# Performance work log

Measured on AMD Instinct MI355X. Metric: run time of the kernel, lower is better.

The kernel has to match this reference:

```python
import jax, jax.numpy as jnp
import numpy as np

B, M, N = 4, 1024, 4096
DQ, DC, H, DH = 512, 512, 8, 64
D = H * DH
NEG = -10000000.0


def setup_inputs() -> dict:
    key = jax.random.key(0)
    ks = jax.random.split(key, 7)
    left = jax.random.normal(ks[0], (B, M, DQ), dtype=jnp.float32)
    right = jax.random.normal(ks[1], (B, N, DC), dtype=jnp.float32)
    mask = jax.random.randint(ks[2], (B, M, N), 0, 2).astype(bool)
    # learned params (torch Linear stores weight as (out,in); we store (in,out))
    Wq = jax.random.normal(ks[3], (DQ, D), dtype=jnp.float32) * (DQ ** -0.5)
    Wkv = jax.random.normal(ks[4], (DC, 2 * D), dtype=jnp.float32) * (DC ** -0.5)
    Wout = jax.random.normal(ks[5], (D, DQ), dtype=jnp.float32) * (D ** -0.5)
    bout = jax.random.normal(ks[6], (DQ,), dtype=jnp.float32) * 0.01
    return {"left": left, "right": right, "mask": mask,
            "Wq": Wq, "Wkv": Wkv, "Wout": Wout, "bout": bout}


def reference(left, right, mask, Wq, Wkv, Wout, bout):
    scale = DH ** -0.5
    q = left @ Wq                      # (B, M, D)
    kv = right @ Wkv                   # (B, N, 2D)
    k, v = jnp.split(kv, 2, axis=-1)   # (B, N, D) each
    q = q.reshape(B, M, H, DH).transpose(0, 2, 1, 3)  # (B, H, M, DH)
    k = k.reshape(B, N, H, DH).transpose(0, 2, 1, 3)  # (B, H, N, DH)
    v = v.reshape(B, N, H, DH).transpose(0, 2, 1, 3)  # (B, H, N, DH)
    sim = scale * jnp.einsum('bhmd,bhnd->bhmn', q, k)  # (B, H, M, N)
    sim = jnp.where(mask[:, None, :, :], sim, NEG)
    attn = jax.nn.softmax(sim, axis=-1)
    out = jnp.einsum('bhmn,bhnd->bhmd', attn, v)       # (B, H, M, DH)
    out = out.transpose(0, 2, 1, 3).reshape(B, M, D)
    return out @ Wout + bout           # (B, M, DQ)
```

## Files before the change

kernel.cpp:

```cpp
#include <hip/hip_runtime.h>

typedef _Float16 f16;
typedef __attribute__((ext_vector_type(8))) _Float16 half8;
typedef __attribute__((ext_vector_type(4))) _Float16 half4;
typedef __attribute__((ext_vector_type(4))) float floatx4;
typedef unsigned int uint32;
typedef __attribute__((ext_vector_type(4))) uint32 uint4v;

#define MFMA16(a, b, c) __builtin_amdgcn_mfma_f32_16x16x32_f16((a), (b), (c), 0, 0, 0)

constexpr int B_ = 4, M_ = 1024, N_ = 4096, DQ_ = 512, DC_ = 512, H_ = 8, DH_ = 64, D_ = 512;
constexpr int KP_ = 576;
constexpr int VP_ = 4224;
constexpr int NSPLIT = 4;
constexpr float QSC_ = 0.18033688011112042f;

typedef __attribute__((address_space(1))) const void glds_g;
typedef __attribute__((address_space(3))) void glds_l;
__device__ __forceinline__ void g2lds16(const void* g, void* l) {
    __builtin_amdgcn_global_load_lds((glds_g*)g, (glds_l*)l, 16, 0, 0);
}

__device__ __forceinline__ void wtr_tile(const float* __restrict__ src, f16* __restrict__ dst,
                                         int Nout, int bx, int by, int tid) {
    __shared__ __align__(16) f16 Ts[64][72];
    const int n0 = bx * 64, k0 = by * 64;
    {
        int kr = tid >> 2, q4 = tid & 3;
        const float* sp = src + (size_t)(k0 + kr) * Nout + n0 + q4 * 16;
        float4 x0 = *(const float4*)(sp + 0), x1 = *(const float4*)(sp + 4);
        float4 x2 = *(const float4*)(sp + 8), x3 = *(const float4*)(sp + 12);
        half8 h0, h1;
        h0[0]=(f16)x0.x; h0[1]=(f16)x0.y; h0[2]=(f16)x0.z; h0[3]=(f16)x0.w;
        h0[4]=(f16)x1.x; h0[5]=(f16)x1.y; h0[6]=(f16)x1.z; h0[7]=(f16)x1.w;
        h1[0]=(f16)x2.x; h1[1]=(f16)x2.y; h1[2]=(f16)x2.z; h1[3]=(f16)x2.w;
        h1[4]=(f16)x3.x; h1[5]=(f16)x3.y; h1[6]=(f16)x3.z; h1[7]=(f16)x3.w;
        *(half8*)&Ts[kr][q4 * 16] = h0;
        *(half8*)&Ts[kr][q4 * 16 + 8] = h1;
    }
    __syncthreads();
    {
        int nr = tid >> 2, q = tid & 3;
        half8 h0, h1;
#pragma unroll
        for (int j = 0; j < 8; j++) { h0[j] = Ts[q * 16 + j][nr]; h1[j] = Ts[q * 16 + 8 + j][nr]; }
        f16* dp = dst + (size_t)(n0 + nr) * 512 + k0 + q * 16;
        *(half8*)(dp + 0) = h0;
        *(half8*)(dp + 8) = h1;
    }
}

__global__ __launch_bounds__(256)
void prep_k(const void* __restrict__ mask, uint32* __restrict__ bits,
            const float* __restrict__ left, f16* __restrict__ leftb,
            const float* __restrict__ right, f16* __restrict__ rightb,
            const float* __restrict__ Wq, f16* __restrict__ wqt,
            const float* __restrict__ Wkv, f16* __restrict__ wkvt,
            const float* __restrict__ Wout, f16* __restrict__ woutt) {
    const int blk = blockIdx.x, tid = threadIdx.x;
    if (blk < 4096) {
        __shared__ int s_bad;
        if (tid == 0) s_bad = 0;
        __syncthreads();
        const uint32* w = (const uint32*)mask + (size_t)blk * 1024;
        int bad = 0;
#pragma unroll
        for (int j = 0; j < 4; j++) bad |= (w[tid * 4 + j] & 0xFFFFFFFEu) != 0u;
        if (bad) s_bad = 1;
        __syncthreads();
        const bool bytes_mode = s_bad != 0;
        uint32 v = 0;
        if (bytes_mode) {
            uint4 x = *(const uint4*)((const unsigned char*)mask + (size_t)blk * 4096 + tid * 16);
            uint32 ws_[4] = {x.x, x.y, x.z, x.w};
#pragma unroll
            for (int k = 0; k < 4; k++)
#pragma unroll
                for (int bb = 0; bb < 4; bb++)
                    v |= (((ws_[k] >> (8 * bb)) & 0xFFu) != 0u ? 1u : 0u) << (k * 4 + bb);
        } else {
            const uint4* p = (const uint4*)((const uint32*)mask + (size_t)blk * 4096 + tid * 16);
            uint4 x0 = p[0], x1 = p[1], x2 = p[2], x3 = p[3];
            uint32 ws_[16] = {x0.x, x0.y, x0.z, x0.w, x1.x, x1.y, x1.z, x1.w,
                              x2.x, x2.y, x2.z, x2.w, x3.x, x3.y, x3.z, x3.w};
#pragma unroll
            for (int k = 0; k < 16; k++) v |= (ws_[k] != 0u ? 1u : 0u) << k;
        }
        uint32 other = (uint32)__shfl_xor((int)v, 1);
        if ((tid & 1) == 0)
            bits[(size_t)blk * 128 + (tid >> 1)] = v | (other << 16);
    } else if (blk < 6144) {
        int i = ((blk - 4096) * 256 + tid) * 4;
        float4 x = *(const float4*)(left + i);
        half4 h; h[0] = (f16)x.x; h[1] = (f16)x.y; h[2] = (f16)x.z; h[3] = (f16)x.w;
        *(half4*)(leftb + i) = h;
    } else if (blk < 14336) {
        int i = ((blk - 6144) * 256 + tid) * 4;
        float4 x = *(const float4*)(right + i);
        half4 h; h[0] = (f16)x.x; h[1] = (f16)x.y; h[2] = (f16)x.z; h[3] = (f16)x.w;
        *(half4*)(rightb + i) = h;
    } else if (blk < 14400) {
        int r = blk - 14336;
        wtr_tile(Wq, wqt, 512, r & 7, r >> 3, tid);
    } else if (blk < 14528) {
        int r = blk - 14400;
        wtr_tile(Wkv, wkvt, 1024, r & 15, r >> 4, tid);
    } else {
        int r = blk - 14528;
        wtr_tile(Wout, woutt, 512, r & 7, r >> 3, tid);
    }
}

__global__ __launch_bounds__(256)
void gemmqkv_k(const f16* __restrict__ leftb, const f16* __restrict__ wqt,
               const f16* __restrict__ rightb, const f16* __restrict__ wkvt,
               f16* __restrict__ qb, f16* __restrict__ kb, f16* __restrict__ vt) {
    __shared__ __align__(16) f16 As[128 * 64];
    __shared__ __align__(16) f16 Bs[128 * 64];
    const int hw = blockIdx.x, tid = threadIdx.x;
    const int lane = tid & 63, wave = tid >> 6;
    const int qd = lane >> 4, l16 = lane & 15;
    const int wm = wave >> 1, wn = wave & 1;

    int mode;
    const f16* A; const f16* Bt; size_t m0, n0;
    if (hw < 1024) {
        const int xcd = hw & 7, slot = hw >> 3;
        const int mi_ = xcd * 16 + (slot & 15);
        const int ni_ = slot >> 4;
        size_t rows = (size_t)mi_ * 128, cols = (size_t)ni_ * 128;
        if (cols < 512) { mode = 0; A = rightb; m0 = rows; Bt = wkvt;   n0 = cols; }
        else            { mode = 1; A = wkvt;   m0 = cols; Bt = rightb; n0 = rows; }
    } else {
        const int r = hw - 1024;
        const int xcd = r & 7, slot = r >> 3;
        const int mi_ = xcd * 4 + (slot & 3);
        const int ni_ = slot >> 2;
        mode = 2; A = leftb; Bt = wqt;
        m0 = (size_t)mi_ * 128; n0 = (size_t)ni_ * 128;
    }

    size_t goff[4];
    f16 *la[4], *lb[4];
#pragma unroll
    for (int i = 0; i < 4; i++) {
        int c = i * 256 + wave * 64 + lane;
        int row = c >> 3, col8 = (c & 7) ^ (row & 7);
        goff[i] = (size_t)row * 512 + col8 * 8;
        la[i] = As + (size_t)(i * 256 + wave * 64) * 8;
        lb[i] = Bs + (size_t)(i * 256 + wave * 64) * 8;
    }
    const f16* Ab = A + m0 * 512;
    const f16* Bb = Bt + n0 * 512;

    floatx4 acc[4][4] = {};

    for (int k0 = 0; k0 < 512; k0 += 64) {
        __syncthreads();
#pragma unroll
        for (int i = 0; i < 4; i++) g2lds16(Ab + goff[i] + k0, la[i]);
#pragma unroll
        for (int i = 0; i < 4; i++) g2lds16(Bb + goff[i] + k0, lb[i]);
        __syncthreads();
#pragma unroll
        for (int kk = 0; kk < 2; kk++) {
            half8 a[4], b[4];
#pragma unroll
            for (int t = 0; t < 4; t++) {
                int rowa = wm * 64 + t * 16 + l16;
                int rowb = wn * 64 + t * 16 + l16;
                int pa8 = ((kk * 4 + qd) ^ (rowa & 7)) * 8;
                int pb8 = ((kk * 4 + qd) ^ (rowb & 7)) * 8;
                a[t] = *(const half8*)&As[rowa * 64 + pa8];
                b[t] = *(const half8*)&Bs[rowb * 64 + pb8];
            }
#pragma unroll
            for (int mt = 0; mt < 4; mt++)
#pragma unroll
                for (int nt = 0; nt < 4; nt++)
                    acc[mt][nt] = MFMA16(a[mt], b[nt], acc[mt][nt]);
        }
    }

#pragma unroll
    for (int mt = 0; mt < 4; mt++)
#pragma unroll
        for (int nt = 0; nt < 4; nt++)
#pragma unroll
            for (int r = 0; r < 4; r++) {
                size_t mi = m0 + wm * 64 + mt * 16 + qd * 4 + r;
                size_t ni = n0 + wn * 64 + nt * 16 + l16;
                float v = acc[mt][nt][r];
                if (mode == 2) {
                    qb[mi * 512 + ni] = (f16)v;
                } else if (mode == 0) {
                    kb[mi * KP_ + ni] = (f16)v;
                } else {
                    int dcol = (int)mi - 512;
                    int hh = dcol >> 6, dh = dcol & 63;
                    size_t bb = ni >> 12, nn = ni & 4095;
                    vt[((bb * H_ + hh) * (size_t)DH_ + dh) * VP_ + nn] = (f16)v;
                }
            }
}

__global__ __launch_bounds__(512, 8)
void attn_k(const f16* __restrict__ Qb, const f16* __restrict__ Kb,
            const f16* __restrict__ Vt, const uint32* __restrict__ mb,
            float* __restrict__ Op, float* __restrict__ Lp) {
    const int tid = threadIdx.x;
    const int lane = tid & 63, wave = tid >> 6;
    const int qd = lane >> 4, l16 = lane & 15;
    const int bh = blockIdx.x, b = bh >> 3, h = bh & 7;
    const int z = blockIdx.z;
    constexpr int iters = N_ / (64 * NSPLIT);
    const int n_base = z * iters * 64;
    const int m_base = blockIdx.y * 128 + wave * 16;

    __shared__ __align__(16) f16 Ks[2][64 * 64];
    __shared__ __align__(16) f16 Vs[2][64 * 64];

    half8 q0, q1;
    {
        const f16* qrow = Qb + ((size_t)(b * M_ + m_base + l16)) * D_ + h * DH_;
        half8 r0 = *(const half8*)(qrow + qd * 8);
        half8 r1 = *(const half8*)(qrow + 32 + qd * 8);
#pragma unroll
        for (int j = 0; j < 8; j++) {
            q0[j] = (f16)((float)r0[j] * QSC_);
            q1[j] = (f16)((float)r1[j] * QSC_);
        }
    }

    floatx4 ot[4] = {};
    float l_acc = 0.0f;

    const uint32* mrow = mb + ((size_t)(b * M_ + m_base + l16)) * (N_ / 32);

    const int srow = wave * 8;
    const int r8 = lane >> 3, p8 = lane & 7;
    const int gc8 = p8 ^ r8;
    const f16* kg = Kb + ((size_t)(b * N_) + srow + r8) * KP_ + h * DH_ + gc8 * 8;
    const f16* vg = Vt + ((size_t)(bh * DH_) + srow + r8) * VP_ + gc8 * 8;

    auto stage = [&](int buf, int n0) {
        g2lds16(kg + (size_t)n0 * KP_, &Ks[buf][srow * 64]);
        g2lds16(vg + n0, &Vs[buf][srow * 64]);
    };

    stage(0, n_base);
    uint2 mmc = *(const uint2*)(mrow + (n_base >> 5));
    int cur = 0;

    const int swz = (l16 & 7);
    const int c0 = (qd ^ swz) * 8;
    const int c1 = ((4 + qd) ^ swz) * 8;

    for (int it = 0; it < iters; it++) {
        const int n0 = n_base + it * 64;
        __syncthreads();
        uint2 mmn;
        if (it + 1 < iters) {
            stage(cur ^ 1, n0 + 64);
            mmn = *(const uint2*)(mrow + ((n0 + 64) >> 5));
        }
        const f16* Kc = &Ks[cur][0];
        const f16* Vc = &Vs[cur][0];

        const uint32 u0 = mmc.x >> (qd * 4);
        const uint32 u1 = mmc.y >> (qd * 4);

        uint32 pk[4][2];
        half8 kc0 = *(const half8*)&Kc[(l16) * 64 + c0];
        half8 kc1 = *(const half8*)&Kc[(l16) * 64 + c1];
#pragma unroll
        for (int s = 0; s < 4; s++) {
            floatx4 t = {};
            t = MFMA16(kc0, q0, t);
            t = MFMA16(kc1, q1, t);
            if (s < 3) {
                const int ro = ((s + 1) * 16 + l16) * 64;
                kc0 = *(const half8*)&Kc[ro + c0];
                kc1 = *(const half8*)&Kc[ro + c1];
            }
            uint32 us = (s & 2 ? u1 : u0) >> ((s & 1) * 16);
            float e0 = __builtin_amdgcn_exp2f(t[0]);
            float e1 = __builtin_amdgcn_exp2f(t[1]);
            float e2 = __builtin_amdgcn_exp2f(t[2]);
            float e3 = __builtin_amdgcn_exp2f(t[3]);
            e0 = (us & 1u) ? e0 : 0.0f;
            e1 = (us & 2u) ? e1 : 0.0f;
            e2 = (us & 4u) ? e2 : 0.0f;
            e3 = (us & 8u) ? e3 : 0.0f;
            l_acc += (e0 + e1) + (e2 + e3);
            pk[s][0] = __builtin_bit_cast(uint32, __builtin_amdgcn_cvt_pkrtz(e0, e1));
            pk[s][1] = __builtin_bit_cast(uint32, __builtin_amdgcn_cvt_pkrtz(e2, e3));
        }

        half8 pa[2];
#pragma unroll
        for (int hh = 0; hh < 2; hh++) {
            uint32 w0, w1, w2, w3;
            {
                auto a = __builtin_amdgcn_permlane32_swap(pk[2 * hh][0], pk[2 * hh + 1][0], false, false);
                auto c = __builtin_amdgcn_permlane16_swap(a[0], a[1], false, false);
                w0 = c[0]; w2 = c[1];
            }
            {
                auto a = __builtin_amdgcn_permlane32_swap(pk[2 * hh][1], pk[2 * hh + 1][1], false, false);
                auto c = __builtin_amdgcn_permlane16_swap(a[0], a[1], false, false);
                w1 = c[0]; w3 = c[1];
            }
            uint4v wv = {w0, w1, w2, w3};
            pa[hh] = __builtin_bit_cast(half8, wv);
        }

        half8 vc0 = *(const half8*)&Vc[(l16) * 64 + c0];
        half8 vc1 = *(const half8*)&Vc[(l16) * 64 + c1];
#pragma unroll
        for (int sd = 0; sd < 4; sd++) {
            floatx4 o = ot[sd];
            o = MFMA16(vc0, pa[0], o);
            o = MFMA16(vc1, pa[1], o);
            if (sd < 3) {
                const int ro = ((sd + 1) * 16 + l16) * 64;
                vc0 = *(const half8*)&Vc[ro + c0];
                vc1 = *(const half8*)&Vc[ro + c1];
            }
            ot[sd] = o;
        }
        mmc = mmn;
        cur ^= 1;
    }

    l_acc += __shfl_xor(l_acc, 16);
    l_acc += __shfl_xor(l_acc, 32);

    {
        size_t row = (size_t)(z * 32 + bh) * M_ + m_base + l16;
        float* op = Op + row * DH_ + qd * 4;
#pragma unroll
        for (int sd = 0; sd < 4; sd++)
            __builtin_nontemporal_store(ot[sd], (floatx4*)(op + sd * 16));
        if (qd == 0) __builtin_nontemporal_store(l_acc, Lp + row);
    }
}

__global__ __launch_bounds__(256)
void comb_k(const float* __restrict__ Op, const float* __restrict__ Lp, f16* __restrict__ Ob,
            int nsp) {
    int i = blockIdx.x * 256 + threadIdx.x;
    int d4 = i & 15, m = (i >> 4) & 1023, bh = i >> 14;
    float nx = 0.f, ny = 0.f, nz = 0.f, nw = 0.f, den = 0.f;
    for (int s = 0; s < nsp; s++) {
        size_t row = ((size_t)s * 32 + bh) * M_ + m;
        float4 x = *(const float4*)(Op + row * DH_ + d4 * 4);
        nx += x.x; ny += x.y; nz += x.z; nw += x.w;
        den += Lp[row];
    }
    float r = 1.0f / den;
    int b = bh >> 3, h = bh & 7;
    f16* o = Ob + ((size_t)(b * M_ + m)) * D_ + h * DH_ + d4 * 4;
    half4 hv; hv[0] = (f16)(nx * r); hv[1] = (f16)(ny * r); hv[2] = (f16)(nz * r); hv[3] = (f16)(nw * r);
    *(half4*)o = hv;
}

__global__ __launch_bounds__(256)
void gemmout_k(const f16* __restrict__ A, const f16* __restrict__ Bt,
               float* __restrict__ Fout, const float* __restrict__ bias) {
    __shared__ __align__(16) f16 As[2][64 * 64];
    __shared__ __align__(16) f16 Bs[2][64 * 64];
    const int tid = threadIdx.x;
    const int lane = tid & 63, wave = tid >> 6;
    const int qd = lane >> 4, l16 = lane & 15;
    const int wm = wave >> 1, wn = wave & 1;
    const size_t m0 = (size_t)blockIdx.x * 64;
    const size_t n0 = (size_t)blockIdx.y * 64;

    size_t goff[2];
    f16 *la[2][2], *lb[2][2];
#pragma unroll
    for (int i = 0; i < 2; i++) {
        int c = i * 256 + wave * 64 + lane;
        int row = c >> 3, col8 = (c & 7) ^ (row & 7);
        goff[i] = (size_t)row * 512 + col8 * 8;
        la[0][i] = &As[0][(size_t)(i * 256 + wave * 64) * 8];
        la[1][i] = &As[1][(size_t)(i * 256 + wave * 64) * 8];
        lb[0][i] = &Bs[0][(size_t)(i * 256 + wave * 64) * 8];
        lb[1][i] = &Bs[1][(size_t)(i * 256 + wave * 64) * 8];
    }
    const f16* Ab = A + m0 * 512;
    const f16* Bb = Bt + n0 * 512;

    floatx4 acc[2][2] = {};

#pragma unroll
    for (int i = 0; i < 2; i++) g2lds16(Ab + goff[i], la[0][i]);
#pragma unroll
    for (int i = 0; i < 2; i++) g2lds16(Bb + goff[i], lb[0][i]);
    int cur = 0;

    for (int k0 = 0; k0 < 512; k0 += 64) {
        __syncthreads();
        if (k0 + 64 < 512) {
            const int nxt = cur ^ 1;
#pragma unroll
            for (int i = 0; i < 2; i++) g2lds16(Ab + goff[i] + k0 + 64, la[nxt][i]);
#pragma unroll
            for (int i = 0; i < 2; i++) g2lds16(Bb + goff[i] + k0 + 64, lb[nxt][i]);
        }
        const f16* Ac = &As[cur][0];
        const f16* Bc = &Bs[cur][0];
#pragma unroll
        for (int kk = 0; kk < 2; kk++) {
            half8 a[2], b[2];
#pragma unroll
            for (int t = 0; t < 2; t++) {
                int rowa = wm * 32 + t * 16 + l16;
                int rowb = wn * 32 + t * 16 + l16;
                int pa8 = ((kk * 4 + qd) ^ (rowa & 7)) * 8;
                int pb8 = ((kk * 4 + qd) ^ (rowb & 7)) * 8;
                a[t] = *(const half8*)&Ac[rowa * 64 + pa8];
                b[t] = *(const half8*)&Bc[rowb * 64 + pb8];
            }
#pragma unroll
            for (int mt = 0; mt < 2; mt++)
#pragma unroll
                for (int nt = 0; nt < 2; nt++)
                    acc[mt][nt] = MFMA16(a[mt], b[nt], acc[mt][nt]);
        }
        cur ^= 1;
    }

#pragma unroll
    for (int mt = 0; mt < 2; mt++)
#pragma unroll
        for (int nt = 0; nt < 2; nt++)
#pragma unroll
            for (int r = 0; r < 4; r++) {
                size_t row = m0 + wm * 32 + mt * 16 + qd * 4 + r;
                size_t col = n0 + wn * 32 + nt * 16 + l16;
                Fout[row * 512 + col] = acc[mt][nt][r] + bias[col];
            }
}

extern "C" void kernel_launch(void* const* d_in, const int* in_sizes, int n_in,
                              void* d_out, int out_size, void* d_ws, size_t ws_size,
                              hipStream_t stream) {
    const float* left  = (const float*)d_in[0];
    const float* right = (const float*)d_in[1];
    const void*  mask  = d_in[2];
    const float* Wq    = (const float*)d_in[3];
    const float* Wkv   = (const float*)d_in[4];
    const float* Wout  = (const float*)d_in[5];
    const float* bout  = (const float*)d_in[6];

    char* ws = (char*)d_ws;
    size_t off = 0;
    auto take = [&](size_t bytes) { char* p = ws + off; off += (bytes + 255) & ~(size_t)255; return p; };
    uint32* mbits = (uint32*)take((size_t)B_ * M_ * N_ / 8);
    f16* woutt = (f16*)take((size_t)D_ * DQ_ * 2);
    f16* qb    = (f16*)take((size_t)B_ * M_ * D_ * 2);
    f16* kb    = (f16*)take((size_t)B_ * N_ * KP_ * 2);
    f16* vt    = (f16*)take((size_t)B_ * H_ * DH_ * VP_ * 2);
    f16* ob    = (f16*)take((size_t)B_ * M_ * D_ * 2);
    char* pool = (char*)take((size_t)34 * 1024 * 1024);
    f16* leftb  = (f16*)pool;
    f16* rightb = (f16*)(pool + (size_t)4 * 1024 * 1024);
    f16* wqt    = (f16*)(pool + (size_t)20 * 1024 * 1024);
    f16* wkvt   = (f16*)(pool + (size_t)21 * 1024 * 1024);
    float* Op   = (float*)pool;
    float* Lp   = (float*)(pool + (size_t)NSPLIT * 32 * M_ * DH_ * 4);

    prep_k<<<14592, 256, 0, stream>>>(mask, mbits, left, leftb, right, rightb,
                                      Wq, wqt, Wkv, wkvt, Wout, woutt);
    gemmqkv_k<<<1152, 256, 0, stream>>>(leftb, wqt, rightb, wkvt, qb, kb, vt);
    attn_k<<<dim3(32, 8, NSPLIT), 512, 0, stream>>>(qb, kb, vt, mbits, Op, Lp);
    comb_k<<<2048, 256, 0, stream>>>(Op, Lp, ob, NSPLIT);
    gemmout_k<<<dim3(64, 8), 256, 0, stream>>>(ob, woutt, (float*)d_out, bout);
}
```

Baseline: 274.9 us.

## Process two 16-row query tiles per wave to reuse K/V LDS fragments

Each wave in the attention kernel now handles 32 query rows as two 16-row fragments instead of 16. Every K and V fragment read from LDS feeds twice as many MFMAs. The grid's M dimension is halved so each block covers 256 rows. This cuts LDS traffic and global K/V staging per query row. In exchange it roughly doubles accumulator and P registers per wave, lowers the launch-bounds occupancy hint from 8 to 4, and halves the number of blocks, which may reduce latency hiding.

```diff
diff --git a/kernel.cpp b/kernel.cpp
--- a/kernel.cpp
+++ b/kernel.cpp
@@ -204,7 +204,7 @@
             }
 }
 
-__global__ __launch_bounds__(512, 8)
+__global__ __launch_bounds__(512, 4)
 void attn_k(const f16* __restrict__ Qb, const f16* __restrict__ Kb,
             const f16* __restrict__ Vt, const uint32* __restrict__ mb,
             float* __restrict__ Op, float* __restrict__ Lp) {
@@ -215,27 +215,29 @@
     const int z = blockIdx.z;
     constexpr int iters = N_ / (64 * NSPLIT);
     const int n_base = z * iters * 64;
-    const int m_base = blockIdx.y * 128 + wave * 16;
+    const int m_base = blockIdx.y * 256 + wave * 32;
 
     __shared__ __align__(16) f16 Ks[2][64 * 64];
     __shared__ __align__(16) f16 Vs[2][64 * 64];
 
-    half8 q0, q1;
-    {
-        const f16* qrow = Qb + ((size_t)(b * M_ + m_base + l16)) * D_ + h * DH_;
+    half8 q[2][2];
+#pragma unroll
+    for (int f = 0; f < 2; f++) {
+        const f16* qrow = Qb + ((size_t)(b * M_ + m_base + f * 16 + l16)) * D_ + h * DH_;
         half8 r0 = *(const half8*)(qrow + qd * 8);
         half8 r1 = *(const half8*)(qrow + 32 + qd * 8);
 #pragma unroll
         for (int j = 0; j < 8; j++) {
-            q0[j] = (f16)((float)r0[j] * QSC_);
-            q1[j] = (f16)((float)r1[j] * QSC_);
-        }
-    }
-
-    floatx4 ot[4] = {};
-    float l_acc = 0.0f;
-
-    const uint32* mrow = mb + ((size_t)(b * M_ + m_base + l16)) * (N_ / 32);
+            q[f][0][j] = (f16)((float)r0[j] * QSC_);
+            q[f][1][j] = (f16)((float)r1[j] * QSC_);
+        }
+    }
+
+    floatx4 ot[2][4] = {};
+    float la0 = 0.0f, la1 = 0.0f;
+
+    const uint32* mrow0 = mb + ((size_t)(b * M_ + m_base + l16)) * (N_ / 32);
+    const uint32* mrow1 = mrow0 + (size_t)16 * (N_ / 32);
 
     const int srow = wave * 8;
     const int r8 = lane >> 3, p8 = lane & 7;
@@ -249,7 +251,8 @@
     };
 
     stage(0, n_base);
-    uint2 mmc = *(const uint2*)(mrow + (n_base >> 5));
+    uint2 mc0 = *(const uint2*)(mrow0 + (n_base >> 5));
+    uint2 mc1 = *(const uint2*)(mrow1 + (n_base >> 5));
     int cur = 0;
 
     const int swz = (l16 & 7);
@@ -259,90 +262,107 @@
     for (int it = 0; it < iters; it++) {
         const int n0 = n_base + it * 64;
         __syncthreads();
-        uint2 mmn;
+        uint2 mn0, mn1;
         if (it + 1 < iters) {
             stage(cur ^ 1, n0 + 64);
-            mmn = *(const uint2*)(mrow + ((n0 + 64) >> 5));
+            mn0 = *(const uint2*)(mrow0 + ((n0 + 64) >> 5));
+            mn1 = *(const uint2*)(mrow1 + ((n0 + 64) >> 5));
         }
         const f16* Kc = &Ks[cur][0];
         const f16* Vc = &Vs[cur][0];
 
-        const uint32 u0 = mmc.x >> (qd * 4);
-        const uint32 u1 = mmc.y >> (qd * 4);
-
-        uint32 pk[4][2];
-        half8 kc0 = *(const half8*)&Kc[(l16) * 64 + c0];
-        half8 kc1 = *(const half8*)&Kc[(l16) * 64 + c1];
+        const uint32 u00 = mc0.x >> (qd * 4), u01 = mc0.y >> (qd * 4);
+        const uint32 u10 = mc1.x >> (qd * 4), u11 = mc1.y >> (qd * 4);
+
+        uint32 pk[2][4][2];
 #pragma unroll
         for (int s = 0; s < 4; s++) {
-            floatx4 t = {};
-            t = MFMA16(kc0, q0, t);
-            t = MFMA16(kc1, q1, t);
-            if (s < 3) {
-                const int ro = ((s + 1) * 16 + l16) * 64;
-                kc0 = *(const half8*)&Kc[ro + c0];
-                kc1 = *(const half8*)&Kc[ro + c1];
-            }
-            uint32 us = (s & 2 ? u1 : u0) >> ((s & 1) * 16);
-            float e0 = __builtin_amdgcn_exp2f(t[0]);
-            float e1 = __builtin_amdgcn_exp2f(t[1]);
-            float e2 = __builtin_amdgcn_exp2f(t[2]);
-            float e3 = __builtin_amdgcn_exp2f(t[3]);
-            e0 = (us & 1u) ? e0 : 0.0f;
-            e1 = (us & 2u) ? e1 : 0.0f;
-            e2 = (us & 4u) ? e2 : 0.0f;
-            e3 = (us & 8u) ? e3 : 0.0f;
-            l_acc += (e0 + e1) + (e2 + e3);
-            pk[s][0] = __builtin_bit_cast(uint32, __builtin_amdgcn_cvt_pkrtz(e0, e1));
-            pk[s][1] = __builtin_bit_cast(uint32, __builtin_amdgcn_cvt_pkrtz(e2, e3));
-        }
-
-        half8 pa[2];
-#pragma unroll
-        for (int hh = 0; hh < 2; hh++) {
-            uint32 w0, w1, w2, w3;
+            const int ro = (s * 16 + l16) * 64;
+            half8 k0 = *(const half8*)&Kc[ro + c0];
+            half8 k1 = *(const half8*)&Kc[ro + c1];
             {
-                auto a = __builtin_amdgcn_permlane32_swap(pk[2 * hh][0], pk[2 * hh + 1][0], false, false);
-                auto c = __builtin_amdgcn_permlane16_swap(a[0], a[1], false, false);
-                w0 = c[0]; w2 = c[1];
+                floatx4 t = {};
+                t = MFMA16(k0, q[0][0], t);
+                t = MFMA16(k1, q[0][1], t);
+                uint32 us = (s & 2 ? u01 : u00) >> ((s & 1) * 16);
+                float e0 = __builtin_amdgcn_exp2f(t[0]);
+                float e1 = __builtin_amdgcn_exp2f(t[1]);
+                float e2 = __builtin_amdgcn_exp2f(t[2]);
+                float e3 = __builtin_amdgcn_exp2f(t[3]);
+                e0 = (us & 1u) ? e0 : 0.0f;
+                e1 = (us & 2u) ? e1 : 0.0f;
+                e2 = (us & 4u) ? e2 : 0.0f;
+                e3 = (us & 8u) ? e3 : 0.0f;
+                la0 += (e0 + e1) + (e2 + e3);
+                pk[0][s][0] = __builtin_bit_cast(uint32, __builtin_amdgcn_cvt_pkrtz(e0, e1));
+                pk[0][s][1] = __builtin_bit_cast(uint32, __builtin_amdgcn_cvt_pkrtz(e2, e3));
             }
             {
-                auto a = __builtin_amdgcn_permlane32_swap(pk[2 * hh][1], pk[2 * hh + 1][1], false, false);
-                auto c = __builtin_amdgcn_permlane16_swap(a[0], a[1], false, false);
-                w1 = c[0]; w3 = c[1];
-            }
-            uint4v wv = {w0, w1, w2, w3};
-            pa[hh] = __builtin_bit_cast(half8, wv);
-        }
-
-        half8 vc0 = *(const half8*)&Vc[(l16) * 64 + c0];
-        half8 vc1 = *(const half8*)&Vc[(l16) * 64 + c1];
+                floatx4 t = {};
+                t = MFMA16(k0, q[1][0], t);
+                t = MFMA16(k1, q[1][1], t);
+                uint32 us = (s & 2 ? u11 : u10) >> ((s & 1) * 16);
+                float e0 = __builtin_amdgcn_exp2f(t[0]);
+                float e1 = __builtin_amdgcn_exp2f(t[1]);
+                float e2 = __builtin_amdgcn_exp2f(t[2]);
+                float e3 = __builtin_amdgcn_exp2f(t[3]);
+                e0 = (us & 1u) ? e0 : 0.0f;
+                e1 = (us & 2u) ? e1 : 0.0f;
+                e2 = (us & 4u) ? e2 : 0.0f;
+                e3 = (us & 8u) ? e3 : 0.0f;
+                la1 += (e0 + e1) + (e2 + e3);
+                pk[1][s][0] = __builtin_bit_cast(uint32, __builtin_amdgcn_cvt_pkrtz(e0, e1));
+                pk[1][s][1] = __builtin_bit_cast(uint32, __builtin_amdgcn_cvt_pkrtz(e2, e3));
+            }
+        }
+
+        half8 pa[2][2];
+#pragma unroll
+        for (int f = 0; f < 2; f++)
+#pragma unroll
+            for (int hh = 0; hh < 2; hh++) {
+                uint32 w0, w1, w2, w3;
+                {
+                    auto a = __builtin_amdgcn_permlane32_swap(pk[f][2 * hh][0], pk[f][2 * hh + 1][0], false, false);
+                    auto c = __builtin_amdgcn_permlane16_swap(a[0], a[1], false, false);
+                    w0 = c[0]; w2 = c[1];
+                }
+                {
+                    auto a = __builtin_amdgcn_permlane32_swap(pk[f][2 * hh][1], pk[f][2 * hh + 1][1], false, false);
+                    auto c = __builtin_amdgcn_permlane16_swap(a[0], a[1], false, false);
+                    w1 = c[0]; w3 = c[1];
+                }
+                uint4v wv = {w0, w1, w2, w3};
+                pa[f][hh] = __builtin_bit_cast(half8, wv);
+            }
+
 #pragma unroll
         for (int sd = 0; sd < 4; sd++) {
-            floatx4 o = ot[sd];
-            o = MFMA16(vc0, pa[0], o);
-            o = MFMA16(vc1, pa[1], o);
-            if (sd < 3) {
-                const int ro = ((sd + 1) * 16 + l16) * 64;
-                vc0 = *(const half8*)&Vc[ro + c0];
-                vc1 = *(const half8*)&Vc[ro + c1];
-            }
-            ot[sd] = o;
-        }
-        mmc = mmn;
+            const int ro = (sd * 16 + l16) * 64;
+            half8 v0 = *(const half8*)&Vc[ro + c0];
+            half8 v1 = *(const half8*)&Vc[ro + c1];
+            ot[0][sd] = MFMA16(v0, pa[0][0], ot[0][sd]);
+            ot[0][sd] = MFMA16(v1, pa[0][1], ot[0][sd]);
+            ot[1][sd] = MFMA16(v0, pa[1][0], ot[1][sd]);
+            ot[1][sd] = MFMA16(v1, pa[1][1], ot[1][sd]);
+        }
+        mc0 = mn0; mc1 = mn1;
         cur ^= 1;
     }
 
-    l_acc += __shfl_xor(l_acc, 16);
-    l_acc += __shfl_xor(l_acc, 32);
-
-    {
-        size_t row = (size_t)(z * 32 + bh) * M_ + m_base + l16;
+    la0 += __shfl_xor(la0, 16);
+    la0 += __shfl_xor(la0, 32);
+    la1 += __shfl_xor(la1, 16);
+    la1 += __shfl_xor(la1, 32);
+
+#pragma unroll
+    for (int f = 0; f < 2; f++) {
+        size_t row = (size_t)(z * 32 + bh) * M_ + m_base + f * 16 + l16;
         float* op = Op + row * DH_ + qd * 4;
 #pragma unroll
         for (int sd = 0; sd < 4; sd++)
-            __builtin_nontemporal_store(ot[sd], (floatx4*)(op + sd * 16));
-        if (qd == 0) __builtin_nontemporal_store(l_acc, Lp + row);
+            __builtin_nontemporal_store(ot[f][sd], (floatx4*)(op + sd * 16));
+        if (qd == 0) __builtin_nontemporal_store(f == 0 ? la0 : la1, Lp + row);
     }
 }
 
@@ -475,7 +495,7 @@
     prep_k<<<14592, 256, 0, stream>>>(mask, mbits, left, leftb, right, rightb,
                                       Wq, wqt, Wkv, wkvt, Wout, woutt);
     gemmqkv_k<<<1152, 256, 0, stream>>>(leftb, wqt, rightb, wkvt, qb, kb, vt);
-    attn_k<<<dim3(32, 8, NSPLIT), 512, 0, stream>>>(qb, kb, vt, mbits, Op, Lp);
+    attn_k<<<dim3(32, 4, NSPLIT), 512, 0, stream>>>(qb, kb, vt, mbits, Op, Lp);
     comb_k<<<2048, 256, 0, stream>>>(Op, Lp, ob, NSPLIT);
     gemmout_k<<<dim3(64, 8), 256, 0, stream>>>(ob, woutt, (float*)d_out, bout);
 }
```

Measured after the change: 273.6 us. Within noise of the previous version (-0.5%).

## Fuse fp32-to-fp16 activation conversion into QKV GEMM with register prefetch

Applied to the files above, without the earlier changes.

Drops the separate conversion passes that wrote fp16 copies of left and right in the prep kernel. The QKV GEMM now reads fp32 activations directly, converts them in registers and writes them into LDS, prefetching the next K-slice into registers while the MFMAs run. It also remaps the block-to-tile assignment for the KV part and simplifies the attention kernel's K/V LDS loads by removing manual software prefetch. This saves a full write and read of the fp16 activation buffers, but doubles the global bytes read for the fp32 operand per GEMM tile and adds register pressure.

```diff
diff --git a/kernel.cpp b/kernel.cpp
--- a/kernel.cpp
+++ b/kernel.cpp
@@ -52,8 +52,6 @@
 
 __global__ __launch_bounds__(256)
 void prep_k(const void* __restrict__ mask, uint32* __restrict__ bits,
-            const float* __restrict__ left, f16* __restrict__ leftb,
-            const float* __restrict__ right, f16* __restrict__ rightb,
             const float* __restrict__ Wq, f16* __restrict__ wqt,
             const float* __restrict__ Wkv, f16* __restrict__ wkvt,
             const float* __restrict__ Wout, f16* __restrict__ woutt) {
@@ -89,31 +87,21 @@
         uint32 other = (uint32)__shfl_xor((int)v, 1);
         if ((tid & 1) == 0)
             bits[(size_t)blk * 128 + (tid >> 1)] = v | (other << 16);
-    } else if (blk < 6144) {
-        int i = ((blk - 4096) * 256 + tid) * 4;
-        float4 x = *(const float4*)(left + i);
-        half4 h; h[0] = (f16)x.x; h[1] = (f16)x.y; h[2] = (f16)x.z; h[3] = (f16)x.w;
-        *(half4*)(leftb + i) = h;
-    } else if (blk < 14336) {
-        int i = ((blk - 6144) * 256 + tid) * 4;
-        float4 x = *(const float4*)(right + i);
-        half4 h; h[0] = (f16)x.x; h[1] = (f16)x.y; h[2] = (f16)x.z; h[3] = (f16)x.w;
-        *(half4*)(rightb + i) = h;
-    } else if (blk < 14400) {
-        int r = blk - 14336;
+    } else if (blk < 4160) {
+        int r = blk - 4096;
         wtr_tile(Wq, wqt, 512, r & 7, r >> 3, tid);
-    } else if (blk < 14528) {
-        int r = blk - 14400;
+    } else if (blk < 4288) {
+        int r = blk - 4160;
         wtr_tile(Wkv, wkvt, 1024, r & 15, r >> 4, tid);
     } else {
-        int r = blk - 14528;
+        int r = blk - 4288;
         wtr_tile(Wout, woutt, 512, r & 7, r >> 3, tid);
     }
 }
 
 __global__ __launch_bounds__(256)
-void gemmqkv_k(const f16* __restrict__ leftb, const f16* __restrict__ wqt,
-               const f16* __restrict__ rightb, const f16* __restrict__ wkvt,
+void gemmqkv_k(const float* __restrict__ left, const f16* __restrict__ wqt,
+               const float* __restrict__ right, const f16* __restrict__ wkvt,
                f16* __restrict__ qb, f16* __restrict__ kb, f16* __restrict__ vt) {
     __shared__ __align__(16) f16 As[128 * 64];
     __shared__ __align__(16) f16 Bs[128 * 64];
@@ -123,45 +111,74 @@
     const int wm = wave >> 1, wn = wave & 1;
 
     int mode;
-    const f16* A; const f16* Bt; size_t m0, n0;
+    const float* F32b; const f16* F16b; size_t m0, n0;
+    bool f32A;
     if (hw < 1024) {
-        const int xcd = hw & 7, slot = hw >> 3;
-        const int mi_ = xcd * 16 + (slot & 15);
-        const int ni_ = slot >> 4;
+        const int xcd = hw & 7, s = hw >> 3;
+        const int mi_ = (s >> 6) * 64 + xcd * 8 + (s & 7);
+        const int ni_ = (s >> 3) & 7;
         size_t rows = (size_t)mi_ * 128, cols = (size_t)ni_ * 128;
-        if (cols < 512) { mode = 0; A = rightb; m0 = rows; Bt = wkvt;   n0 = cols; }
-        else            { mode = 1; A = wkvt;   m0 = cols; Bt = rightb; n0 = rows; }
+        F32b = right + rows * 512;
+        F16b = wkvt + cols * 512;
+        if (cols < 512) { mode = 0; f32A = true;  m0 = rows; n0 = cols; }
+        else            { mode = 1; f32A = false; m0 = cols; n0 = rows; }
     } else {
         const int r = hw - 1024;
-        const int xcd = r & 7, slot = r >> 3;
-        const int mi_ = xcd * 4 + (slot & 3);
-        const int ni_ = slot >> 2;
-        mode = 2; A = leftb; Bt = wqt;
+        const int xcd = r & 7, s = r >> 3;
+        const int mi_ = xcd * 4 + (s & 3);
+        const int ni_ = s >> 2;
+        mode = 2; f32A = true;
         m0 = (size_t)mi_ * 128; n0 = (size_t)ni_ * 128;
-    }
-
-    size_t goff[4];
-    f16 *la[4], *lb[4];
+        F32b = left + m0 * 512;
+        F16b = wqt + n0 * 512;
+    }
+    f16* LF32 = f32A ? As : Bs;
+    f16* LF16 = f32A ? Bs : As;
+
+    int crow[4], ccol8[4];
+    size_t g16off[4];
+    f16* g16dst[4];
 #pragma unroll
     for (int i = 0; i < 4; i++) {
         int c = i * 256 + wave * 64 + lane;
         int row = c >> 3, col8 = (c & 7) ^ (row & 7);
-        goff[i] = (size_t)row * 512 + col8 * 8;
-        la[i] = As + (size_t)(i * 256 + wave * 64) * 8;
-        lb[i] = Bs + (size_t)(i * 256 + wave * 64) * 8;
-    }
-    const f16* Ab = A + m0 * 512;
-    const f16* Bb = Bt + n0 * 512;
+        crow[i] = row; ccol8[i] = col8;
+        g16off[i] = (size_t)row * 512 + col8 * 8;
+        g16dst[i] = LF16 + (size_t)(i * 256 + wave * 64) * 8;
+    }
 
     floatx4 acc[4][4] = {};
+    float4 ra[4][2];
+
+#pragma unroll
+    for (int i = 0; i < 4; i++) {
+        const float* sp = F32b + (size_t)crow[i] * 512 + ccol8[i] * 8;
+        ra[i][0] = *(const float4*)sp;
+        ra[i][1] = *(const float4*)(sp + 4);
+    }
 
     for (int k0 = 0; k0 < 512; k0 += 64) {
         __syncthreads();
 #pragma unroll
-        for (int i = 0; i < 4; i++) g2lds16(Ab + goff[i] + k0, la[i]);
-#pragma unroll
-        for (int i = 0; i < 4; i++) g2lds16(Bb + goff[i] + k0, lb[i]);
-        __syncthreads();
+        for (int i = 0; i < 4; i++) g2lds16(F16b + g16off[i] + k0, g16dst[i]);
+#pragma unroll
+        for (int i = 0; i < 4; i++) {
+            half8 hh;
+            hh[0] = (f16)ra[i][0].x; hh[1] = (f16)ra[i][0].y;
+            hh[2] = (f16)ra[i][0].z; hh[3] = (f16)ra[i][0].w;
+            hh[4] = (f16)ra[i][1].x; hh[5] = (f16)ra[i][1].y;
+            hh[6] = (f16)ra[i][1].z; hh[7] = (f16)ra[i][1].w;
+            *(half8*)&LF32[(size_t)(i * 256 + wave * 64 + lane) * 8] = hh;
+        }
+        __syncthreads();
+        if (k0 + 64 < 512) {
+#pragma unroll
+            for (int i = 0; i < 4; i++) {
+                const float* sp = F32b + (size_t)crow[i] * 512 + (k0 + 64) + ccol8[i] * 8;
+                ra[i][0] = *(const float4*)sp;
+                ra[i][1] = *(const float4*)(sp + 4);
+            }
+        }
 #pragma unroll
         for (int kk = 0; kk < 2; kk++) {
             half8 a[4], b[4];
@@ -253,8 +270,6 @@
     int cur = 0;
 
     const int swz = (l16 & 7);
-    const int c0 = (qd ^ swz) * 8;
-    const int c1 = ((4 + qd) ^ swz) * 8;
 
     for (int it = 0; it < iters; it++) {
         const int n0 = n_base + it * 64;
@@ -264,25 +279,19 @@
             stage(cur ^ 1, n0 + 64);
             mmn = *(const uint2*)(mrow + ((n0 + 64) >> 5));
         }
-        const f16* Kc = &Ks[cur][0];
-        const f16* Vc = &Vs[cur][0];
 
         const uint32 u0 = mmc.x >> (qd * 4);
         const uint32 u1 = mmc.y >> (qd * 4);
 
         uint32 pk[4][2];
-        half8 kc0 = *(const half8*)&Kc[(l16) * 64 + c0];
-        half8 kc1 = *(const half8*)&Kc[(l16) * 64 + c1];
 #pragma unroll
         for (int s = 0; s < 4; s++) {
+            const int ro = (s * 16 + l16) * 64;
+            half8 k0 = *(const half8*)&Ks[cur][ro + ((qd ^ swz) * 8)];
+            half8 k1 = *(const half8*)&Ks[cur][ro + (((4 + qd) ^ swz) * 8)];
             floatx4 t = {};
-            t = MFMA16(kc0, q0, t);
-            t = MFMA16(kc1, q1, t);
-            if (s < 3) {
-                const int ro = ((s + 1) * 16 + l16) * 64;
-                kc0 = *(const half8*)&Kc[ro + c0];
-                kc1 = *(const half8*)&Kc[ro + c1];
-            }
+            t = MFMA16(k0, q0, t);
+            t = MFMA16(k1, q1, t);
             uint32 us = (s & 2 ? u1 : u0) >> ((s & 1) * 16);
             float e0 = __builtin_amdgcn_exp2f(t[0]);
             float e1 = __builtin_amdgcn_exp2f(t[1]);
@@ -315,19 +324,13 @@
             pa[hh] = __builtin_bit_cast(half8, wv);
         }
 
-        half8 vc0 = *(const half8*)&Vc[(l16) * 64 + c0];
-        half8 vc1 = *(const half8*)&Vc[(l16) * 64 + c1];
 #pragma unroll
         for (int sd = 0; sd < 4; sd++) {
-            floatx4 o = ot[sd];
-            o = MFMA16(vc0, pa[0], o);
-            o = MFMA16(vc1, pa[1], o);
-            if (sd < 3) {
-                const int ro = ((sd + 1) * 16 + l16) * 64;
-                vc0 = *(const half8*)&Vc[ro + c0];
-                vc1 = *(const half8*)&Vc[ro + c1];
-            }
-            ot[sd] = o;
+            const int ro = (sd * 16 + l16) * 64;
+            half8 v0 = *(const half8*)&Vs[cur][ro + ((qd ^ swz) * 8)];
+            half8 v1 = *(const half8*)&Vs[cur][ro + (((4 + qd) ^ swz) * 8)];
+            ot[sd] = MFMA16(v0, pa[0], ot[sd]);
+            ot[sd] = MFMA16(v1, pa[1], ot[sd]);
         }
         mmc = mmn;
         cur ^= 1;
@@ -465,16 +468,13 @@
     f16* vt    = (f16*)take((size_t)B_ * H_ * DH_ * VP_ * 2);
     f16* ob    = (f16*)take((size_t)B_ * M_ * D_ * 2);
     char* pool = (char*)take((size_t)34 * 1024 * 1024);
-    f16* leftb  = (f16*)pool;
-    f16* rightb = (f16*)(pool + (size_t)4 * 1024 * 1024);
-    f16* wqt    = (f16*)(pool + (size_t)20 * 1024 * 1024);
-    f16* wkvt   = (f16*)(pool + (size_t)21 * 1024 * 1024);
+    f16* wqt    = (f16*)pool;
+    f16* wkvt   = (f16*)(pool + (size_t)1 * 1024 * 1024);
     float* Op   = (float*)pool;
     float* Lp   = (float*)(pool + (size_t)NSPLIT * 32 * M_ * DH_ * 4);
 
-    prep_k<<<14592, 256, 0, stream>>>(mask, mbits, left, leftb, right, rightb,
-                                      Wq, wqt, Wkv, wkvt, Wout, woutt);
-    gemmqkv_k<<<1152, 256, 0, stream>>>(leftb, wqt, rightb, wkvt, qb, kb, vt);
+    prep_k<<<4352, 256, 0, stream>>>(mask, mbits, Wq, wqt, Wkv, wkvt, Wout, woutt);
+    gemmqkv_k<<<1152, 256, 0, stream>>>(left, wqt, right, wkvt, qb, kb, vt);
     attn_k<<<dim3(32, 8, NSPLIT), 512, 0, stream>>>(qb, kb, vt, mbits, Op, Lp);
     comb_k<<<2048, 256, 0, stream>>>(Op, Lp, ob, NSPLIT);
     gemmout_k<<<dim3(64, 8), 256, 0, stream>>>(ob, woutt, (float*)d_out, bout);
```

After: 266.5 us. 3.0% less time.
